# Optimization experiments

Measured on AMD Instinct MI355X. Metric: run time of the kernel, lower is better.

## Reference

```python
import jax, jax.numpy as jnp
import numpy as np


def setup_inputs() -> dict:
    key = jax.random.key(0)
    k1, k2, k3, k4 = jax.random.split(key, 4)
    B, S, D, V, NSEG = 8, 4096, 256, 50257, 16
    tokens = jax.random.randint(k1, (B, S), 0, V, dtype=jnp.int64) if jax.config.jax_enable_x64 else jax.random.randint(k1, (B, S), 0, V).astype(jnp.int32)
    lengths = jax.random.randint(k2, (B,), 1, S + 1).astype(tokens.dtype)
    tok_emb = jax.random.normal(k3, (V, D), dtype=jnp.float32)
    seg_emb = jax.random.normal(k4, (NSEG, D), dtype=jnp.float32)
    return {"tok_emb": tok_emb, "seg_emb": seg_emb, "tokens": tokens,
            "lengths": lengths, "sep_i": 3}


def reference(tok_emb, seg_emb, tokens, lengths, sep_i):
    # tokens: [B, S] padded ragged batch; lengths: [B]
    B, S = tokens.shape
    mask = jnp.arange(S)[None, :] < lengths[:, None]          # [B, S] valid positions
    # segment id = inclusive cumsum of (token == <sep>) within each valid prefix
    seg = jnp.cumsum(((tokens == sep_i) & mask).astype(jnp.int32), axis=1)  # [B, S]
    out = tok_emb[tokens] + seg_emb[seg]                       # [B, S, D]
    # zero out padded positions (packed-sequence equivalent on a padded buffer)
    return out * mask[..., None].astype(out.dtype)
```

## Files before the change

### kernel.cpp

```cpp
#include <hip/hip_runtime.h>

typedef float f32x4 __attribute__((ext_vector_type(4)));
typedef int   i32x4 __attribute__((ext_vector_type(4)));

template <int TP>
__global__ __launch_bounds__(256) void fused_embed_kernel(
        const f32x4* __restrict__ tok_emb,
        const f32x4* __restrict__ seg_emb,
        const int* __restrict__ tokens,
        const int* __restrict__ lengths,
        const int* __restrict__ sep_p,
        f32x4* __restrict__ out,
        int S, int nseg, int V) {
    const int tid  = threadIdx.x;
    const int lane = tid & 63;
    const int wave = tid >> 6;
    const int tiles_per_row = S / TP;
    const int b    = blockIdx.x / tiles_per_row;
    const int p0   = (blockIdx.x % tiles_per_row) * TP;
    const int sep  = sep_p[0];
    const int len  = lengths[b];
    const int* trow = tokens + (size_t)b * S;

    __shared__ int wsum[4];
    __shared__ int seg_lds[TP];
    __shared__ int tok_lds[TP];

    int cnt = 0;
    for (int i = tid * 4; i < p0; i += 1024) {
        const i32x4 t4 = *reinterpret_cast<const i32x4*>(trow + i);
        cnt += (t4.x == sep && i + 0 < len) ? 1 : 0;
        cnt += (t4.y == sep && i + 1 < len) ? 1 : 0;
        cnt += (t4.z == sep && i + 2 < len) ? 1 : 0;
        cnt += (t4.w == sep && i + 3 < len) ? 1 : 0;
    }
    #pragma unroll
    for (int off = 32; off; off >>= 1) cnt += __shfl_xor(cnt, off);
    if (lane == 0) wsum[wave] = cnt;
    __syncthreads();
    const int P0 = wsum[0] + wsum[1] + wsum[2] + wsum[3];

    if (wave == 0 && lane < TP) {
        const int s = p0 + lane;
        const int t = trow[s];
        int inc = (t == sep && s < len) ? 1 : 0;
        #pragma unroll
        for (int off = 1; off < TP; off <<= 1) {
            int up = __shfl_up(inc, off);
            if (lane >= off) inc += up;
        }
        int sg = P0 + inc;
        if (sg >= nseg) sg = nseg - 1;
        seg_lds[lane] = (s < len) ? sg : -1;
        tok_lds[lane] = (t < 0) ? 0 : ((t >= V) ? V - 1 : t);
    }
    __syncthreads();

    const size_t out_base = ((size_t)b * S + p0) * 64;
    #pragma unroll
    for (int k = 0; k < TP / 4; ++k) {
        const int pi = wave + k * 4;
        const int sg = seg_lds[pi];
        f32x4 r = (f32x4)0.f;
        if (sg >= 0) {
            const int t = tok_lds[pi];
            const f32x4 a = tok_emb[((size_t)t  << 6) + lane];
            const f32x4 e = seg_emb[((size_t)sg << 6) + lane];
            r = a + e;
        }
        __builtin_nontemporal_store(r, &out[out_base + (size_t)pi * 64 + lane]);
    }
}

__global__ __launch_bounds__(1024) void seg_scan_kernel(
        const int* __restrict__ tokens,
        const int* __restrict__ lengths,
        const int* __restrict__ sep_p,
        int* __restrict__ seg,
        int S) {
    const int b    = blockIdx.x;
    const int tid  = threadIdx.x;
    const int lane = tid & 63;
    const int wave = tid >> 6;
    const int sep  = sep_p[0];
    const int len  = lengths[b];
    const int* trow = tokens + (size_t)b * S;
    int* srow       = seg    + (size_t)b * S;

    __shared__ int wsum[16];
    __shared__ int carry_s;
    if (tid == 0) carry_s = 0;

    const int CHUNK = 4096;
    for (int base = 0; base < S; base += CHUNK) {
        const int s0 = base + tid * 4;
        int t0 = 0, t1 = 0, t2 = 0, t3 = 0;
        if (s0 + 3 < S) {
            const i32x4 t4 = *reinterpret_cast<const i32x4*>(trow + s0);
            t0 = t4.x; t1 = t4.y; t2 = t4.z; t3 = t4.w;
        } else {
            if (s0 + 0 < S) t0 = trow[s0 + 0];
            if (s0 + 1 < S) t1 = trow[s0 + 1];
            if (s0 + 2 < S) t2 = trow[s0 + 2];
            if (s0 + 3 < S) t3 = trow[s0 + 3];
        }
        int v0 = ((t0 == sep) && (s0 + 0 < len)) ? 1 : 0;
        int v1 = v0 + (((t1 == sep) && (s0 + 1 < len)) ? 1 : 0);
        int v2 = v1 + (((t2 == sep) && (s0 + 2 < len)) ? 1 : 0);
        int v3 = v2 + (((t3 == sep) && (s0 + 3 < len)) ? 1 : 0);
        const int cnt = v3;

        int ws = cnt;
        #pragma unroll
        for (int off = 1; off < 64; off <<= 1) {
            int up = __shfl_up(ws, off);
            if (lane >= off) ws += up;
        }
        if (lane == 63) wsum[wave] = ws;
        __syncthreads();

        int wave_excl = 0, total = 0;
        #pragma unroll
        for (int w = 0; w < 16; ++w) {
            int t = wsum[w];
            if (w < wave) wave_excl += t;
            total += t;
        }
        const int carry = carry_s;
        const int excl  = carry + wave_excl + (ws - cnt);

        if (s0 + 3 < S && s0 + 4 <= len) {
            i32x4 o; o.x = excl + v0; o.y = excl + v1; o.z = excl + v2; o.w = excl + v3;
            *reinterpret_cast<i32x4*>(srow + s0) = o;
        } else {
            if (s0 + 0 < S) srow[s0 + 0] = (s0 + 0 < len) ? excl + v0 : -1;
            if (s0 + 1 < S) srow[s0 + 1] = (s0 + 1 < len) ? excl + v1 : -1;
            if (s0 + 2 < S) srow[s0 + 2] = (s0 + 2 < len) ? excl + v2 : -1;
            if (s0 + 3 < S) srow[s0 + 3] = (s0 + 3 < len) ? excl + v3 : -1;
        }
        __syncthreads();
        if (tid == 0) carry_s = carry + total;
    }
}

__global__ __launch_bounds__(256) void gather_add_div_kernel(
        const f32x4* __restrict__ tok_emb,
        const f32x4* __restrict__ seg_emb,
        const int* __restrict__ tokens,
        const int* __restrict__ seg,
        f32x4* __restrict__ out,
        int D4, int nseg, int V, long long total) {
    const long long tid = (long long)blockIdx.x * blockDim.x + threadIdx.x;
    if (tid >= total) return;
    const int lane = (int)(tid % D4);
    const long long pos = tid / D4;

    const int sg_raw = seg[pos];
    f32x4 r = (f32x4)0.f;
    if (sg_raw >= 0) {
        int t = tokens[pos];
        t = (t < 0) ? 0 : ((t >= V) ? V - 1 : t);
        int sg = (sg_raw >= nseg) ? nseg - 1 : sg_raw;
        const f32x4 a = tok_emb[(size_t)t * D4 + lane];
        const f32x4 e = seg_emb[(size_t)sg * D4 + lane];
        r = a + e;
    }
    __builtin_nontemporal_store(r, &out[(size_t)pos * D4 + lane]);
}

extern "C" void kernel_launch(void* const* d_in, const int* in_sizes, int n_in,
                              void* d_out, int out_size, void* d_ws, size_t ws_size,
                              hipStream_t stream) {
    const float* tok_emb = (const float*)d_in[0];
    const float* seg_emb = (const float*)d_in[1];
    const int*   tokens  = (const int*)d_in[2];
    const int*   lengths = (const int*)d_in[3];
    const int*   sep_p   = (const int*)d_in[4];

    const int B    = in_sizes[3];
    const int BS   = in_sizes[2];
    const int S    = BS / B;
    const int D    = out_size / BS;
    const int nseg = in_sizes[1] / D;
    const int V    = in_sizes[0] / D;
    const int D4   = D / 4;

    constexpr int TP = 16;
    if (D4 == 64 && (S % TP) == 0) {
        const int grid = BS / TP;
        fused_embed_kernel<TP><<<grid, 256, 0, stream>>>(
            (const f32x4*)tok_emb, (const f32x4*)seg_emb,
            tokens, lengths, sep_p, (f32x4*)d_out, S, nseg, V);
    } else {
        int* seg_ws = (int*)d_ws;
        seg_scan_kernel<<<B, 1024, 0, stream>>>(tokens, lengths, sep_p, seg_ws, S);
        const long long total = (long long)BS * D4;
        const int block = 256;
        const int grid  = (int)((total + block - 1) / block);
        gather_add_div_kernel<<<grid, block, 0, stream>>>(
            (const f32x4*)tok_emb, (const f32x4*)seg_emb,
            tokens, seg_ws, (f32x4*)d_out, D4, nseg, V, total);
    }
}
```

Measured before the change: 13.00 us.

## Prefetch token embedding rows before the segment scan and enlarge the tile

```diff
diff --git a/kernel.cpp b/kernel.cpp
--- a/kernel.cpp
+++ b/kernel.cpp
@@ -4,7 +4,7 @@
 typedef int   i32x4 __attribute__((ext_vector_type(4)));
 
 template <int TP>
-__global__ __launch_bounds__(256) void fused_embed_kernel(
+__global__ __launch_bounds__(256) void fused_embed_v2(
         const f32x4* __restrict__ tok_emb,
         const f32x4* __restrict__ seg_emb,
         const int* __restrict__ tokens,
@@ -12,20 +12,31 @@
         const int* __restrict__ sep_p,
         f32x4* __restrict__ out,
         int S, int nseg, int V) {
+    constexpr int PW = TP / 4;
     const int tid  = threadIdx.x;
     const int lane = tid & 63;
     const int wave = tid >> 6;
-    const int tiles_per_row = S / TP;
-    const int b    = blockIdx.x / tiles_per_row;
-    const int p0   = (blockIdx.x % tiles_per_row) * TP;
+    const int tiles = S / TP;
+    const int b    = blockIdx.x / tiles;
+    const int tile = (tiles - 1) - (blockIdx.x % tiles);
+    const int p0   = tile * TP;
     const int sep  = sep_p[0];
     const int len  = lengths[b];
     const int* trow = tokens + (size_t)b * S;
 
+    int tk[PW];
+    #pragma unroll
+    for (int k = 0; k < PW; ++k) tk[k] = trow[p0 + wave + k * 4];
+    f32x4 a[PW];
+    #pragma unroll
+    for (int k = 0; k < PW; ++k) {
+        int t = tk[k];
+        t = (t < 0) ? 0 : ((t >= V) ? V - 1 : t);
+        a[k] = tok_emb[((size_t)t << 6) + lane];
+    }
+
     __shared__ int wsum[4];
     __shared__ int seg_lds[TP];
-    __shared__ int tok_lds[TP];
-
     int cnt = 0;
     for (int i = tid * 4; i < p0; i += 1024) {
         const i32x4 t4 = *reinterpret_cast<const i32x4*>(trow + i);
@@ -52,23 +63,17 @@
         int sg = P0 + inc;
         if (sg >= nseg) sg = nseg - 1;
         seg_lds[lane] = (s < len) ? sg : -1;
-        tok_lds[lane] = (t < 0) ? 0 : ((t >= V) ? V - 1 : t);
     }
     __syncthreads();
 
-    const size_t out_base = ((size_t)b * S + p0) * 64;
-    #pragma unroll
-    for (int k = 0; k < TP / 4; ++k) {
+    const size_t out_base = ((size_t)b * S + p0) * 64 + lane;
+    #pragma unroll
+    for (int k = 0; k < PW; ++k) {
         const int pi = wave + k * 4;
         const int sg = seg_lds[pi];
         f32x4 r = (f32x4)0.f;
-        if (sg >= 0) {
-            const int t = tok_lds[pi];
-            const f32x4 a = tok_emb[((size_t)t  << 6) + lane];
-            const f32x4 e = seg_emb[((size_t)sg << 6) + lane];
-            r = a + e;
-        }
-        __builtin_nontemporal_store(r, &out[out_base + (size_t)pi * 64 + lane]);
+        if (sg >= 0) r = a[k] + seg_emb[((size_t)sg << 6) + lane];
+        __builtin_nontemporal_store(r, &out[out_base + (size_t)pi * 64]);
     }
 }
 
@@ -185,10 +190,10 @@
     const int V    = in_sizes[0] / D;
     const int D4   = D / 4;
 
-    constexpr int TP = 16;
+    constexpr int TP = 32;
     if (D4 == 64 && (S % TP) == 0) {
         const int grid = BS / TP;
-        fused_embed_kernel<TP><<<grid, 256, 0, stream>>>(
+        fused_embed_v2<TP><<<grid, 256, 0, stream>>>(
             (const f32x4*)tok_emb, (const f32x4*)seg_emb,
             tokens, lengths, sep_p, (f32x4*)d_out, S, nseg, V);
     } else {
```

After: 15.26 us. 1.17x slower.

## Precompute per-tile separator prefix counts in a separate pass

Applied to the files above, without the earlier changes.

```diff
diff --git a/kernel.cpp b/kernel.cpp
--- a/kernel.cpp
+++ b/kernel.cpp
@@ -3,44 +3,72 @@
 typedef float f32x4 __attribute__((ext_vector_type(4)));
 typedef int   i32x4 __attribute__((ext_vector_type(4)));
 
+__global__ __launch_bounds__(64) void tile_count_kernel(
+        const int* __restrict__ tokens,
+        const int* __restrict__ lengths,
+        const int* __restrict__ sep_p,
+        int* __restrict__ chunkTot,
+        int* __restrict__ tilePre,
+        int S, int nchunk) {
+    const int lane = threadIdx.x;
+    const int b    = blockIdx.x / nchunk;
+    const int c    = blockIdx.x % nchunk;
+    const int sep  = sep_p[0];
+    const int len  = lengths[b];
+    const int* trow = tokens + (size_t)b * S;
+    const int s0 = c * 1024 + lane * 16;
+
+    int cnt = 0;
+    #pragma unroll
+    for (int k = 0; k < 4; ++k) {
+        const int si = s0 + k * 4;
+        const i32x4 t4 = *reinterpret_cast<const i32x4*>(trow + si);
+        cnt += (t4.x == sep && si + 0 < len) ? 1 : 0;
+        cnt += (t4.y == sep && si + 1 < len) ? 1 : 0;
+        cnt += (t4.z == sep && si + 2 < len) ? 1 : 0;
+        cnt += (t4.w == sep && si + 3 < len) ? 1 : 0;
+    }
+    int inc = cnt;
+    #pragma unroll
+    for (int off = 1; off < 64; off <<= 1) {
+        int up = __shfl_up(inc, off);
+        if (lane >= off) inc += up;
+    }
+    tilePre[(size_t)blockIdx.x * 64 + lane] = inc - cnt;
+    if (lane == 63) chunkTot[blockIdx.x] = inc;
+}
+
 template <int TP>
-__global__ __launch_bounds__(256) void fused_embed_kernel(
+__global__ __launch_bounds__(256) void fused_embed_v3(
         const f32x4* __restrict__ tok_emb,
         const f32x4* __restrict__ seg_emb,
         const int* __restrict__ tokens,
         const int* __restrict__ lengths,
         const int* __restrict__ sep_p,
+        const int* __restrict__ chunkTot,
+        const int* __restrict__ tilePre,
         f32x4* __restrict__ out,
-        int S, int nseg, int V) {
+        int S, int nseg, int V, int nchunk) {
     const int tid  = threadIdx.x;
     const int lane = tid & 63;
     const int wave = tid >> 6;
     const int tiles_per_row = S / TP;
     const int b    = blockIdx.x / tiles_per_row;
-    const int p0   = (blockIdx.x % tiles_per_row) * TP;
+    const int tile = blockIdx.x % tiles_per_row;
+    const int p0   = tile * TP;
     const int sep  = sep_p[0];
     const int len  = lengths[b];
     const int* trow = tokens + (size_t)b * S;
 
-    __shared__ int wsum[4];
     __shared__ int seg_lds[TP];
     __shared__ int tok_lds[TP];
 
-    int cnt = 0;
-    for (int i = tid * 4; i < p0; i += 1024) {
-        const i32x4 t4 = *reinterpret_cast<const i32x4*>(trow + i);
-        cnt += (t4.x == sep && i + 0 < len) ? 1 : 0;
-        cnt += (t4.y == sep && i + 1 < len) ? 1 : 0;
-        cnt += (t4.z == sep && i + 2 < len) ? 1 : 0;
-        cnt += (t4.w == sep && i + 3 < len) ? 1 : 0;
-    }
-    #pragma unroll
-    for (int off = 32; off; off >>= 1) cnt += __shfl_xor(cnt, off);
-    if (lane == 0) wsum[wave] = cnt;
-    __syncthreads();
-    const int P0 = wsum[0] + wsum[1] + wsum[2] + wsum[3];
-
+    const int c   = p0 >> 10;
+    const int tin = (p0 >> 4) & 63;
     if (wave == 0 && lane < TP) {
+        int base = tilePre[((size_t)(b * nchunk + c)) * 64 + tin];
+        for (int cc = 0; cc < c; ++cc) base += chunkTot[b * nchunk + cc];
+
         const int s = p0 + lane;
         const int t = trow[s];
         int inc = (t == sep && s < len) ? 1 : 0;
@@ -49,14 +77,14 @@
             int up = __shfl_up(inc, off);
             if (lane >= off) inc += up;
         }
-        int sg = P0 + inc;
+        int sg = base + inc;
         if (sg >= nseg) sg = nseg - 1;
         seg_lds[lane] = (s < len) ? sg : -1;
         tok_lds[lane] = (t < 0) ? 0 : ((t >= V) ? V - 1 : t);
     }
     __syncthreads();
 
-    const size_t out_base = ((size_t)b * S + p0) * 64;
+    const size_t out_base = ((size_t)b * S + p0) * 64 + lane;
     #pragma unroll
     for (int k = 0; k < TP / 4; ++k) {
         const int pi = wave + k * 4;
@@ -68,7 +96,7 @@
             const f32x4 e = seg_emb[((size_t)sg << 6) + lane];
             r = a + e;
         }
-        __builtin_nontemporal_store(r, &out[out_base + (size_t)pi * 64 + lane]);
+        __builtin_nontemporal_store(r, &out[out_base + (size_t)pi * 64]);
     }
 }
 
@@ -186,11 +214,19 @@
     const int D4   = D / 4;
 
     constexpr int TP = 16;
-    if (D4 == 64 && (S % TP) == 0) {
+    if (D4 == 64 && (S % 1024) == 0) {
+        const int nchunk = S / 1024;
+        int* chunkTot = (int*)d_ws;
+        int* tilePre  = chunkTot + B * nchunk;
+
+        tile_count_kernel<<<B * nchunk, 64, 0, stream>>>(
+            tokens, lengths, sep_p, chunkTot, tilePre, S, nchunk);
+
         const int grid = BS / TP;
-        fused_embed_kernel<TP><<<grid, 256, 0, stream>>>(
+        fused_embed_v3<TP><<<grid, 256, 0, stream>>>(
             (const f32x4*)tok_emb, (const f32x4*)seg_emb,
-            tokens, lengths, sep_p, (f32x4*)d_out, S, nseg, V);
+            tokens, lengths, sep_p, chunkTot, tilePre,
+            (f32x4*)d_out, S, nseg, V, nchunk);
     } else {
         int* seg_ws = (int*)d_ws;
         seg_scan_kernel<<<B, 1024, 0, stream>>>(tokens, lengths, sep_p, seg_ws, S);
```

Measured after the change: 17.70 us. 1.36x slower.
